# Kernel optimization log

Hardware: AMD Instinct MI355X
Metric: run time of the kernel (lower is better)

The kernel has to match this reference:

```python
import jax, jax.numpy as jnp
import numpy as np

B, N, C, NH = 4, 4096, 192, 3
H = W = 64
HD = C // NH  # 64
K_SPA = [8, 4, 2]
SCALE = C ** (-0.5)
LN_EPS = 1e-5


def _ln(x, g, b):
    m = jnp.mean(x, axis=-1, keepdims=True)
    v = jnp.mean(jnp.square(x - m), axis=-1, keepdims=True)
    return (x - m) * jax.lax.rsqrt(v + LN_EPS) * g + b


def _conv2d(x, w, b, padding='VALID', groups=1):
    y = jax.lax.conv_general_dilated(
        x, w, window_strides=(1, 1), padding=padding,
        dimension_numbers=('NCHW', 'OIHW', 'NCHW'), feature_group_count=groups)
    return y + b[None, :, None, None]


def _branch(x_img, q_h, kv_w, kv_b, sr_w, sr_b, ln_g, ln_b, lc_w, lc_b):
    # x_img: [B,C,H,W]; q_h: [B,N,HD]
    f = _conv2d(x_img, sr_w, sr_b)                      # [B,C,h',w'] (VALID, stride 1)
    m = f.shape[2] * f.shape[3]
    side = f.shape[2]                                   # square: h'==w'
    t = f.reshape(B, C, m).transpose(0, 2, 1)           # [B,m,C]
    t = jax.nn.gelu(_ln(t, ln_g, ln_b), approximate=False)
    kv = (t @ kv_w.T + kv_b).reshape(B, m, NH, HD)      # head-split of kv proj
    k = kv[:, :, 0, :]                                  # [B,m,HD] (head 0 -> k)
    v = kv[:, :, 1, :]                                  # [B,m,HD] (head 1 -> v)
    attn = jax.nn.softmax(jnp.einsum('bnd,bmd->bnm', q_h, k) * SCALE, axis=-1)
    v_img = v.transpose(0, 2, 1).reshape(B, HD, side, side)
    v = v + _conv2d(v_img, lc_w, lc_b, padding=((1, 1), (1, 1)), groups=HD)\
        .reshape(B, HD, m).transpose(0, 2, 1)           # local depthwise conv added to V
    return jnp.einsum('bnm,bmd->bnd', attn, v)          # [B,N,HD]


def _fwd(x, q_w, q_b, kv_w, kv_b, sr1_w, sr1_b, sr2_w, sr2_b, sr3_w, sr3_b,
         ln1_g, ln1_b, ln2_g, ln2_b, ln3_g, ln3_b,
         lc1_w, lc1_b, lc2_w, lc2_b, lc3_w, lc3_b, nn1_w, nn1_b):
    q = (x @ q_w.T + q_b).reshape(B, N, NH, HD).transpose(0, 2, 1, 3)  # [B,NH,N,HD]
    x_img = x.transpose(0, 2, 1).reshape(B, C, H, W)
    x1 = _branch(x_img, q[:, 0], kv_w, kv_b, sr1_w, sr1_b, ln1_g, ln1_b, lc1_w, lc1_b)
    x2 = _branch(x_img, q[:, 1], kv_w, kv_b, sr2_w, sr2_b, ln2_g, ln2_b, lc2_w, lc2_b)
    x3 = _branch(x_img, q[:, 2], kv_w, kv_b, sr3_w, sr3_b, ln3_g, ln3_b, lc3_w, lc3_b)
    out = jnp.concatenate([x1, x2, x3], axis=-1)        # [B,N,C]
    return out @ nn1_w.T + nn1_b


def setup_inputs() -> dict:
    key = jax.random.key(0)
    ks = jax.random.split(key, 16)
    s = lambda i, shp: (jax.random.normal(ks[i], shp, jnp.float32) * 0.02)
    d = dict(
        x=jax.random.normal(ks[0], (B, N, C), jnp.float32),
        q_w=s(1, (C, C)), q_b=jnp.zeros((C,), jnp.float32),
        kv_w=s(2, (C, C)), kv_b=jnp.zeros((C,), jnp.float32),
        sr1_w=s(3, (C, C, K_SPA[0], K_SPA[0])), sr1_b=jnp.zeros((C,), jnp.float32),
        sr2_w=s(4, (C, C, K_SPA[1], K_SPA[1])), sr2_b=jnp.zeros((C,), jnp.float32),
        sr3_w=s(5, (C, C, K_SPA[2], K_SPA[2])), sr3_b=jnp.zeros((C,), jnp.float32),
        ln1_g=jnp.ones((C,), jnp.float32), ln1_b=jnp.zeros((C,), jnp.float32),
        ln2_g=jnp.ones((C,), jnp.float32), ln2_b=jnp.zeros((C,), jnp.float32),
        ln3_g=jnp.ones((C,), jnp.float32), ln3_b=jnp.zeros((C,), jnp.float32),
        lc1_w=s(6, (HD, 1, 3, 3)), lc1_b=jnp.zeros((HD,), jnp.float32),
        lc2_w=s(7, (HD, 1, 3, 3)), lc2_b=jnp.zeros((HD,), jnp.float32),
        lc3_w=s(8, (HD, 1, 3, 3)), lc3_b=jnp.zeros((HD,), jnp.float32),
        nn1_w=s(9, (C, C)), nn1_b=jnp.zeros((C,), jnp.float32),
    )
    return d


def reference(x, q_w, q_b, kv_w, kv_b, sr1_w, sr1_b, sr2_w, sr2_b, sr3_w, sr3_b,
              ln1_g, ln1_b, ln2_g, ln2_b, ln3_g, ln3_b,
              lc1_w, lc1_b, lc2_w, lc2_b, lc3_w, lc3_b, nn1_w, nn1_b):
    return _fwd(x, q_w, q_b, kv_w, kv_b, sr1_w, sr1_b, sr2_w, sr2_b, sr3_w, sr3_b,
                ln1_g, ln1_b, ln2_g, ln2_b, ln3_g, ln3_b,
                lc1_w, lc1_b, lc2_w, lc2_b, lc3_w, lc3_b, nn1_w, nn1_b)
```

## Files before the change

### kernel.cpp

```cpp
#include <hip/hip_runtime.h>
#include <hip/hip_bf16.h>

typedef unsigned short u16;
typedef unsigned int   u32;
typedef __attribute__((ext_vector_type(8))) short bf16x8;
typedef __attribute__((ext_vector_type(4))) float f32x4;

#define DI static __device__ __forceinline__
#define MFMA(a,b,c) __builtin_amdgcn_mfma_f32_16x16x32_bf16(a,b,c,0,0,0)

static constexpr int CB = 192;
static constexpr int NB = 4096;
static constexpr int BB = 4;
static constexpr float SCALE = 0.07216878364870323f;

DI float b2f(u16 u){ union{u32 i; float f;} x; x.i = (u32)u << 16; return x.f; }
DI u16 f2b(float f){ union{u32 i; float f;} x; x.f = f;
  u32 r = x.i + 0x7FFFu + ((x.i >> 16) & 1u); return (u16)(r >> 16); }

DI int swzb(int row, int byteInRow){ return row*128 + (byteInRow ^ ((row & 7) << 4)); }

template<bool F32>
DI void stage16(const void* base, size_t eoff, char* dst, int srow, int q4){
  if (F32){
    const float* s = (const float*)base + eoff;
    float4 a0 = *(const float4*)(s);
    float4 a1 = *(const float4*)(s + 4);
    float4 a2 = *(const float4*)(s + 8);
    float4 a3 = *(const float4*)(s + 12);
    union { uint4 v; u16 h[8]; } r0, r1;
    r0.h[0]=f2b(a0.x); r0.h[1]=f2b(a0.y); r0.h[2]=f2b(a0.z); r0.h[3]=f2b(a0.w);
    r0.h[4]=f2b(a1.x); r0.h[5]=f2b(a1.y); r0.h[6]=f2b(a1.z); r0.h[7]=f2b(a1.w);
    r1.h[0]=f2b(a2.x); r1.h[1]=f2b(a2.y); r1.h[2]=f2b(a2.z); r1.h[3]=f2b(a2.w);
    r1.h[4]=f2b(a3.x); r1.h[5]=f2b(a3.y); r1.h[6]=f2b(a3.z); r1.h[7]=f2b(a3.w);
    *(uint4*)(dst + swzb(srow, q4*32))      = r0.v;
    *(uint4*)(dst + swzb(srow, q4*32 + 16)) = r1.v;
  } else {
    const u16* s = (const u16*)base + eoff;
    *(uint4*)(dst + swzb(srow, q4*32))      = *(const uint4*)(s);
    *(uint4*)(dst + swzb(srow, q4*32 + 16)) = *(const uint4*)(s + 8);
  }
}

__global__ __launch_bounds__(256) void cvt_k(const float* __restrict__ in,
      u16* __restrict__ out, int n4){
  int i = blockIdx.x*256 + threadIdx.x;
  if (i >= n4) return;
  float4 v = ((const float4*)in)[i];
  union{ uint2 u; u16 h[4]; } r;
  r.h[0]=f2b(v.x); r.h[1]=f2b(v.y); r.h[2]=f2b(v.z); r.h[3]=f2b(v.w);
  ((uint2*)out)[i] = r.u;
}

template<int K>
__global__ void repack_k(const float* __restrict__ w, u16* __restrict__ wt, int total){
  int i = blockIdx.x*256 + threadIdx.x;
  if (i >= total) return;
  int kk  = i / (CB*CB);
  int rem = i % (CB*CB);
  int co = rem / CB, ci = rem % CB;
  int ky = kk / K, kx = kk % K;
  wt[i] = f2b(w[((co*CB + ci)*K + ky)*K + kx]);
}

template<int K>
__global__ __launch_bounds__(256) void conv_k(const u16* __restrict__ xb,
      const u16* __restrict__ wt, const float* __restrict__ bias,
      u16* __restrict__ out, int side, int m){
  constexpr int AR = K*64;
  __shared__ char lds[(AR + 2*192)*128];
  char* Awin = lds;
  char* W0 = lds + AR*128;
  char* W1 = W0 + 192*128;

  const int t = threadIdx.x;
  const int w = t >> 6, l = t & 63, lr = l & 15, lg = l >> 4;
  const int b = blockIdx.x / side;
  const int oy = blockIdx.x % side;

  int boff[12][2];
  #pragma unroll
  for (int f = 0; f < 12; ++f){
    boff[f][0] = swzb(16*f + lr, lg*16);
    boff[f][1] = swzb(16*f + lr, 64 + lg*16);
  }

  f32x4 zero = {0.f,0.f,0.f,0.f};
  f32x4 acc[12];
  #pragma unroll
  for (int f = 0; f < 12; ++f) acc[f] = zero;

  const int rowb = 16*w + lr;
  const int scol = t >> 2, sq4 = t & 3;

  for (int c0 = 0; c0 < CB; c0 += 64){
    __syncthreads();
    #pragma unroll
    for (int r = 0; r < K; ++r){
      stage16<false>(xb, ((size_t)(b*NB + (oy + r)*64 + scol))*CB + c0 + sq4*16,
                     Awin, r*64 + scol, sq4);
    }
    #pragma unroll
    for (int k = 0; k < 3; ++k){
      int s = t + k*256, row = s >> 2, q4 = s & 3;
      stage16<false>(wt, ((size_t)row)*CB + c0 + q4*16, W0, row, q4);
    }
    for (int kk = 0; kk < K*K; ++kk){
      __syncthreads();
      char* Wcur = (kk & 1) ? W1 : W0;
      if (kk + 1 < K*K){
        char* Wnxt = (kk & 1) ? W0 : W1;
        #pragma unroll
        for (int k = 0; k < 3; ++k){
          int s = t + k*256, row = s >> 2, q4 = s & 3;
          stage16<false>(wt, ((size_t)(kk+1)*CB + row)*CB + c0 + q4*16, Wnxt, row, q4);
        }
      }
      int ky = kk / K, kx = kk - ky*K;
      int arow = ky*64 + rowb + kx;
      int x16 = (arow & 7) << 4;
      const char* ab = Awin + arow*128;
      bf16x8 a0 = *(const bf16x8*)(ab + ((lg*16) ^ x16));
      bf16x8 a1 = *(const bf16x8*)(ab + ((64 + lg*16) ^ x16));
      #pragma unroll
      for (int f = 0; f < 12; ++f){
        bf16x8 b0v = *(const bf16x8*)(Wcur + boff[f][0]);
        bf16x8 b1v = *(const bf16x8*)(Wcur + boff[f][1]);
        acc[f] = MFMA(a0, b0v, acc[f]);
        acc[f] = MFMA(a1, b1v, acc[f]);
      }
    }
  }

  const int posb = oy*side;
  #pragma unroll
  for (int f = 0; f < 12; ++f){
    int co = 16*f + lr;
    float bv = bias[co];
    #pragma unroll
    for (int r = 0; r < 4; ++r){
      int ox = 16*w + lg*4 + r;
      if (ox < side)
        out[((size_t)(b*m + posb + ox))*CB + co] = f2b(acc[f][r] + bv);
    }
  }
}

struct GemmP {
  const void* A; const void* W; const float* bias;
  u16* outb; u16* outk; u16* outv; float* outf;
  int Mtot;
  int m;
  int mtiles, ntiles;
};

template<int EPI, bool AF32, bool WF32>
__global__ __launch_bounds__(256) void gemm_k(GemmP p){
  __shared__ uint4 ldsbuf[1024];
  char* ldsA = (char*)ldsbuf;
  char* ldsB = ldsA + 8192;

  const int t = threadIdx.x;
  const int w = t >> 6, l = t & 63, lr = l & 15, lg = l >> 4;

  int bid = blockIdx.x;
  int nt = bid % p.ntiles, mt = bid / p.ntiles;

  const int srow = t >> 2;
  const int q4   = t & 3;

  size_t abase;
  { int row = mt*64 + srow; if (row > p.Mtot - 1) row = p.Mtot - 1;
    abase = (size_t)row * CB; }
  const int wrow = nt*64 + srow;

  const int aoff0 = swzb(16*w + lr, lg*16);
  const int aoff1 = swzb(16*w + lr, 64 + lg*16);
  int boff[4][2];
  #pragma unroll
  for (int f = 0; f < 4; ++f){ boff[f][0] = swzb(16*f + lr, lg*16); boff[f][1] = swzb(16*f + lr, 64 + lg*16); }

  f32x4 zero = {0.f,0.f,0.f,0.f};
  f32x4 acc[4] = {zero, zero, zero, zero};

  size_t wbase = (size_t)wrow * CB;
  for (int c0 = 0; c0 < CB; c0 += 64){
    stage16<AF32>(p.A, abase + c0 + q4*16, ldsA, srow, q4);
    stage16<WF32>(p.W, wbase + c0 + q4*16, ldsB, srow, q4);
    __syncthreads();
    bf16x8 a0 = *(const bf16x8*)(ldsA + aoff0);
    bf16x8 a1 = *(const bf16x8*)(ldsA + aoff1);
    #pragma unroll
    for (int f = 0; f < 4; ++f){
      bf16x8 b0 = *(const bf16x8*)(ldsB + boff[f][0]);
      bf16x8 b1 = *(const bf16x8*)(ldsB + boff[f][1]);
      acc[f] = MFMA(a0, b0, acc[f]);
      acc[f] = MFMA(a1, b1, acc[f]);
    }
    __syncthreads();
  }

  #pragma unroll
  for (int f = 0; f < 4; ++f){
    #pragma unroll
    for (int r = 0; r < 4; ++r){
      int rowt = 16*w + lg*4 + r;
      int col  = nt*64 + 16*f + lr;
      float v = acc[f][r] + p.bias[col];
      int grow = mt*64 + rowt;
      if (grow >= p.Mtot) continue;
      if (EPI == 0){
        p.outb[(size_t)grow*CB + col] = f2b(v);
      } else if (EPI == 2){
        int bb = grow / p.m, pp = grow % p.m;
        if (col < 64) p.outk[(size_t)(bb*p.m + pp)*64 + col]        = f2b(v);
        else          p.outv[(size_t)(bb*p.m + pp)*64 + (col - 64)] = f2b(v);
      } else {
        p.outf[(size_t)grow*CB + col] = v;
      }
    }
  }
}

__global__ __launch_bounds__(256) void ln_gelu_k(const u16* __restrict__ tp,
      const float* __restrict__ g, const float* __restrict__ bt,
      u16* __restrict__ out, int rows){
  int w = threadIdx.x >> 6, l = threadIdx.x & 63;
  int p = blockIdx.x*4 + w;
  if (p >= rows) return;
  const u16* rp = tp + (size_t)p*CB;
  float x0 = b2f(rp[l]), x1 = b2f(rp[l+64]), x2 = b2f(rp[l+128]);
  float s = x0 + x1 + x2;
  #pragma unroll
  for (int d = 1; d < 64; d <<= 1) s += __shfl_xor(s, d);
  float mean = s * (1.0f/192.0f);
  float d0 = x0-mean, d1 = x1-mean, d2 = x2-mean;
  float q = d0*d0 + d1*d1 + d2*d2;
  #pragma unroll
  for (int d = 1; d < 64; d <<= 1) q += __shfl_xor(q, d);
  float rstd = rsqrtf(q * (1.0f/192.0f) + 1e-5f);
  u16* op = out + (size_t)p*CB;
  float dv[3] = {d0, d1, d2};
  #pragma unroll
  for (int i = 0; i < 3; ++i){
    int c = l + i*64;
    float xv = dv[i] * rstd * g[c] + bt[c];
    float ge = 0.5f * xv * (1.0f + erff(xv * 0.7071067811865475f));
    op[c] = f2b(ge);
  }
}

__global__ __launch_bounds__(256) void lcconv_k(const u16* __restrict__ vpre,
      const float* __restrict__ lw, const float* __restrict__ lb,
      u16* __restrict__ vt, int m, int mpad, int side){
  int w = threadIdx.x >> 6, d = threadIdx.x & 63;
  int idx = blockIdx.x*4 + w;
  if (idx >= BB*m) return;
  int b = idx / m, p = idx % m;
  int h = p / side, x = p % side;
  float acc = b2f(vpre[(size_t)idx*64 + d]);
  float wv[9];
  #pragma unroll
  for (int j = 0; j < 9; ++j) wv[j] = lw[d*9 + j];
  #pragma unroll
  for (int dy = 0; dy < 3; ++dy){
    int hh = h + dy - 1;
    if (hh < 0 || hh >= side) continue;
    #pragma unroll
    for (int dx = 0; dx < 3; ++dx){
      int ww = x + dx - 1;
      if (ww < 0 || ww >= side) continue;
      acc += b2f(vpre[(size_t)(b*m + hh*side + ww)*64 + d]) * wv[dy*3 + dx];
    }
  }
  acc += lb[d];
  vt[(size_t)(b*64 + d)*mpad + p] = f2b(acc);
}

__global__ __launch_bounds__(256) void attn_k(const u16* __restrict__ qall,
      const u16* __restrict__ kbuf, const u16* __restrict__ vt,
      u16* __restrict__ xh, int m, int mpad, int head){
  __shared__ uint4 lds[2048];
  char* Qb = (char*)lds;
  char* Kb = Qb + 8192;
  char* Vb = Kb + 8192;
  const int t = threadIdx.x;
  const int w = t >> 6, l = t & 63, lr = l & 15, lg = l >> 4;
  char* Pb = Vb + 8192 + w*2048;
  const int b = blockIdx.x >> 6, q0 = (blockIdx.x & 63)*64;

  {
    int row = t >> 2, seg = (t & 3)*32;
    const char* src = (const char*)(qall + (size_t)(b*NB + q0 + row)*CB + head*64) + seg;
    *(uint4*)(Qb + swzb(row, seg))    = *(const uint4*)src;
    *(uint4*)(Qb + swzb(row, seg+16)) = *(const uint4*)(src + 16);
  }

  const int qoff0 = swzb(16*w + lr, lg*16), qoff1 = swzb(16*w + lr, 64 + lg*16);
  int koff[4][2];
  #pragma unroll
  for (int f = 0; f < 4; ++f){ koff[f][0] = swzb(16*f + lr, lg*16); koff[f][1] = swzb(16*f + lr, 64 + lg*16); }
  const int poff0 = swzb(lr, lg*16), poff1 = swzb(lr, 64 + lg*16);

  float mrow[4] = {-1e30f,-1e30f,-1e30f,-1e30f};
  float lrow[4] = {0.f,0.f,0.f,0.f};
  f32x4 zero = {0.f,0.f,0.f,0.f};
  f32x4 oacc[4] = {zero, zero, zero, zero};

  const int nkc = (m + 63) / 64;
  for (int kc = 0; kc < nkc; ++kc){
    const int j0 = kc*64;
    __syncthreads();
    {
      int j = t >> 2, seg = (t & 3)*32;
      int jj = j0 + j; if (jj > m-1) jj = m-1;
      const char* src = (const char*)(kbuf + (size_t)(b*m + jj)*64) + seg;
      *(uint4*)(Kb + swzb(j, seg))    = *(const uint4*)src;
      *(uint4*)(Kb + swzb(j, seg+16)) = *(const uint4*)(src + 16);
      int d = j;
      const char* sv = (const char*)(vt + (size_t)(b*64 + d)*mpad + j0) + seg;
      *(uint4*)(Vb + swzb(d, seg))    = *(const uint4*)sv;
      *(uint4*)(Vb + swzb(d, seg+16)) = *(const uint4*)(sv + 16);
    }
    __syncthreads();

    f32x4 s[4] = {zero, zero, zero, zero};
    bf16x8 a0 = *(const bf16x8*)(Qb + qoff0);
    bf16x8 a1 = *(const bf16x8*)(Qb + qoff1);
    #pragma unroll
    for (int f = 0; f < 4; ++f){
      bf16x8 k0 = *(const bf16x8*)(Kb + koff[f][0]);
      bf16x8 k1 = *(const bf16x8*)(Kb + koff[f][1]);
      s[f] = MFMA(a0, k0, s[f]);
      s[f] = MFMA(a1, k1, s[f]);
    }
    float fac[4];
    #pragma unroll
    for (int r = 0; r < 4; ++r){
      float mx = -1e30f;
      #pragma unroll
      for (int f = 0; f < 4; ++f){
        float sv = s[f][r] * SCALE;
        int key = j0 + 16*f + lr;
        sv = (key < m) ? sv : -1e30f;
        s[f][r] = sv;
        mx = fmaxf(mx, sv);
      }
      mx = fmaxf(mx, __shfl_xor(mx, 1));
      mx = fmaxf(mx, __shfl_xor(mx, 2));
      mx = fmaxf(mx, __shfl_xor(mx, 4));
      mx = fmaxf(mx, __shfl_xor(mx, 8));
      float mold = mrow[r];
      float mnew = fmaxf(mold, mx);
      mrow[r] = mnew;
      fac[r] = __expf(mold - mnew);
      float rs = 0.f;
      #pragma unroll
      for (int f = 0; f < 4; ++f){
        float pe = __expf(s[f][r] - mnew);
        rs += pe;
        int prow = lg*4 + r, pcol = 16*f + lr;
        *(u16*)(Pb + swzb(prow, pcol*2)) = f2b(pe);
      }
      rs += __shfl_xor(rs, 1);
      rs += __shfl_xor(rs, 2);
      rs += __shfl_xor(rs, 4);
      rs += __shfl_xor(rs, 8);
      lrow[r] = lrow[r]*fac[r] + rs;
    }
    #pragma unroll
    for (int f = 0; f < 4; ++f){
      oacc[f][0] *= fac[0]; oacc[f][1] *= fac[1];
      oacc[f][2] *= fac[2]; oacc[f][3] *= fac[3];
    }
    __syncthreads();
    bf16x8 p0 = *(const bf16x8*)(Pb + poff0);
    bf16x8 p1 = *(const bf16x8*)(Pb + poff1);
    #pragma unroll
    for (int f = 0; f < 4; ++f){
      bf16x8 v0 = *(const bf16x8*)(Vb + koff[f][0]);
      bf16x8 v1 = *(const bf16x8*)(Vb + koff[f][1]);
      oacc[f] = MFMA(p0, v0, oacc[f]);
      oacc[f] = MFMA(p1, v1, oacc[f]);
    }
  }

  #pragma unroll
  for (int f = 0; f < 4; ++f){
    #pragma unroll
    for (int r = 0; r < 4; ++r){
      int row = q0 + 16*w + lg*4 + r;
      int col = head*64 + 16*f + lr;
      xh[(size_t)(b*NB + row)*CB + col] = f2b(oacc[f][r] / lrow[r]);
    }
  }
}

extern "C" void kernel_launch(void* const* d_in, const int* in_sizes, int n_in,
                              void* d_out, int out_size, void* d_ws, size_t ws_size,
                              hipStream_t stream){
  const float* x     = (const float*)d_in[0];
  const float* q_w   = (const float*)d_in[1];
  const float* q_b   = (const float*)d_in[2];
  const float* kv_w  = (const float*)d_in[3];
  const float* kv_b  = (const float*)d_in[4];
  const float* sr_w[3] = {(const float*)d_in[5], (const float*)d_in[7], (const float*)d_in[9]};
  const float* sr_b[3] = {(const float*)d_in[6], (const float*)d_in[8], (const float*)d_in[10]};
  const float* ln_g[3] = {(const float*)d_in[11], (const float*)d_in[13], (const float*)d_in[15]};
  const float* ln_b[3] = {(const float*)d_in[12], (const float*)d_in[14], (const float*)d_in[16]};
  const float* lc_w[3] = {(const float*)d_in[17], (const float*)d_in[19], (const float*)d_in[21]};
  const float* lc_b[3] = {(const float*)d_in[18], (const float*)d_in[20], (const float*)d_in[22]};
  const float* nn1_w = (const float*)d_in[23];
  const float* nn1_b = (const float*)d_in[24];

  char* ws = (char*)d_ws;
  u16* q_all  = (u16*)d_out;
  u16* xb     = (u16*)(ws);
  u16* xheads = (u16*)(ws + 6291456);
  u16* wt     = (u16*)(ws + 12582912);
  u16* kbuf   = (u16*)(ws + 12582912);
  u16* vpre   = (u16*)(ws + 14615040);
  u16* tpre   = (u16*)(ws + 17301504);
  u16* vtb    = (u16*)(ws + 17301504);
  u16* tbuf   = (u16*)(ws + 23397888);

  const int Ks[3] = {8, 4, 2}, sides[3] = {57, 61, 63};

  cvt_k<<<3072, 256, 0, stream>>>(x, xb, 786432);

  {
    GemmP p{}; p.A = xb; p.W = q_w; p.bias = q_b; p.outb = q_all;
    p.Mtot = BB*NB; p.m = BB*NB; p.mtiles = 256; p.ntiles = 3;
    gemm_k<0,false,true><<<256*3, 256, 0, stream>>>(p);
  }

  for (int i = 0; i < 3; ++i){
    const int K = Ks[i], side = sides[i], m = side*side;
    const int mpad = ((m + 64 + 7)/8)*8;
    const int tot = CB*CB*K*K;
    if (i == 0) repack_k<8><<<(tot+255)/256, 256, 0, stream>>>(sr_w[i], wt, tot);
    if (i == 1) repack_k<4><<<(tot+255)/256, 256, 0, stream>>>(sr_w[i], wt, tot);
    if (i == 2) repack_k<2><<<(tot+255)/256, 256, 0, stream>>>(sr_w[i], wt, tot);

    if (i == 0) conv_k<8><<<BB*side, 256, 0, stream>>>(xb, wt, sr_b[i], tpre, side, m);
    if (i == 1) conv_k<4><<<BB*side, 256, 0, stream>>>(xb, wt, sr_b[i], tpre, side, m);
    if (i == 2) conv_k<2><<<BB*side, 256, 0, stream>>>(xb, wt, sr_b[i], tpre, side, m);

    ln_gelu_k<<<m, 256, 0, stream>>>(tpre, ln_g[i], ln_b[i], tbuf, BB*m);

    GemmP pk{}; pk.A = tbuf; pk.W = kv_w; pk.bias = kv_b; pk.outk = kbuf; pk.outv = vpre;
    pk.Mtot = BB*m; pk.m = m; pk.mtiles = (BB*m + 63)/64; pk.ntiles = 2;
    gemm_k<2,false,true><<<pk.mtiles*2, 256, 0, stream>>>(pk);

    lcconv_k<<<m, 256, 0, stream>>>(vpre, lc_w[i], lc_b[i], vtb, m, mpad, side);

    attn_k<<<BB*64, 256, 0, stream>>>(q_all, kbuf, vtb, xheads, m, mpad, i);
  }

  {
    GemmP p{}; p.A = xheads; p.W = nn1_w; p.bias = nn1_b; p.outf = (float*)d_out;
    p.Mtot = BB*NB; p.m = BB*NB; p.mtiles = 256; p.ntiles = 3;
    gemm_k<3,false,true><<<256*3, 256, 0, stream>>>(p);
  }
}
```

Measured before the change: 790.6 us.

## Double block size in conv and attention kernels, splitting work across wave groups

```diff
diff --git a/kernel.cpp b/kernel.cpp
--- a/kernel.cpp
+++ b/kernel.cpp
@@ -64,7 +64,7 @@
 }
 
 template<int K>
-__global__ __launch_bounds__(256) void conv_k(const u16* __restrict__ xb,
+__global__ __launch_bounds__(512) void conv_k(const u16* __restrict__ xb,
       const u16* __restrict__ wt, const float* __restrict__ bias,
       u16* __restrict__ out, int side, int m){
   constexpr int AR = K*64;
@@ -74,36 +74,44 @@
   char* W1 = W0 + 192*128;
 
   const int t = threadIdx.x;
-  const int w = t >> 6, l = t & 63, lr = l & 15, lg = l >> 4;
+  const int l = t & 63, lr = l & 15, lg = l >> 4;
+  const int ww = (t >> 6) & 3, wg = t >> 8;
   const int b = blockIdx.x / side;
   const int oy = blockIdx.x % side;
 
-  int boff[12][2];
-  #pragma unroll
-  for (int f = 0; f < 12; ++f){
-    boff[f][0] = swzb(16*f + lr, lg*16);
-    boff[f][1] = swzb(16*f + lr, 64 + lg*16);
+  int boff[6][2];
+  #pragma unroll
+  for (int f = 0; f < 6; ++f){
+    boff[f][0] = swzb(96*wg + 16*f + lr, lg*16);
+    boff[f][1] = swzb(96*wg + 16*f + lr, 64 + lg*16);
   }
 
   f32x4 zero = {0.f,0.f,0.f,0.f};
-  f32x4 acc[12];
-  #pragma unroll
-  for (int f = 0; f < 12; ++f) acc[f] = zero;
-
-  const int rowb = 16*w + lr;
-  const int scol = t >> 2, sq4 = t & 3;
+  f32x4 acc[6];
+  #pragma unroll
+  for (int f = 0; f < 6; ++f) acc[f] = zero;
+
+  const int rowb = 16*ww + lr;
 
   for (int c0 = 0; c0 < CB; c0 += 64){
     __syncthreads();
     #pragma unroll
-    for (int r = 0; r < K; ++r){
-      stage16<false>(xb, ((size_t)(b*NB + (oy + r)*64 + scol))*CB + c0 + sq4*16,
-                     Awin, r*64 + scol, sq4);
-    }
-    #pragma unroll
-    for (int k = 0; k < 3; ++k){
-      int s = t + k*256, row = s >> 2, q4 = s & 3;
-      stage16<false>(wt, ((size_t)row)*CB + c0 + q4*16, W0, row, q4);
+    for (int k = 0; k < (K*256 + 511)/512; ++k){
+      int s = t + k*512;
+      if (s < K*256){
+        int row = s >> 2, q4 = s & 3;
+        int r = row >> 6, scol = row & 63;
+        stage16<false>(xb, ((size_t)(b*NB + (oy + r)*64 + scol))*CB + c0 + q4*16,
+                       Awin, row, q4);
+      }
+    }
+    #pragma unroll
+    for (int k = 0; k < 2; ++k){
+      int s = t + k*512;
+      if (s < 768){
+        int row = s >> 2, q4 = s & 3;
+        stage16<false>(wt, ((size_t)row)*CB + c0 + q4*16, W0, row, q4);
+      }
     }
     for (int kk = 0; kk < K*K; ++kk){
       __syncthreads();
@@ -111,9 +119,12 @@
       if (kk + 1 < K*K){
         char* Wnxt = (kk & 1) ? W0 : W1;
         #pragma unroll
-        for (int k = 0; k < 3; ++k){
-          int s = t + k*256, row = s >> 2, q4 = s & 3;
-          stage16<false>(wt, ((size_t)(kk+1)*CB + row)*CB + c0 + q4*16, Wnxt, row, q4);
+        for (int k = 0; k < 2; ++k){
+          int s = t + k*512;
+          if (s < 768){
+            int row = s >> 2, q4 = s & 3;
+            stage16<false>(wt, ((size_t)(kk+1)*CB + row)*CB + c0 + q4*16, Wnxt, row, q4);
+          }
         }
       }
       int ky = kk / K, kx = kk - ky*K;
@@ -123,7 +134,7 @@
       bf16x8 a0 = *(const bf16x8*)(ab + ((lg*16) ^ x16));
       bf16x8 a1 = *(const bf16x8*)(ab + ((64 + lg*16) ^ x16));
       #pragma unroll
-      for (int f = 0; f < 12; ++f){
+      for (int f = 0; f < 6; ++f){
         bf16x8 b0v = *(const bf16x8*)(Wcur + boff[f][0]);
         bf16x8 b1v = *(const bf16x8*)(Wcur + boff[f][1]);
         acc[f] = MFMA(a0, b0v, acc[f]);
@@ -134,12 +145,12 @@
 
   const int posb = oy*side;
   #pragma unroll
-  for (int f = 0; f < 12; ++f){
-    int co = 16*f + lr;
+  for (int f = 0; f < 6; ++f){
+    int co = 96*wg + 16*f + lr;
     float bv = bias[co];
     #pragma unroll
     for (int r = 0; r < 4; ++r){
-      int ox = 16*w + lg*4 + r;
+      int ox = 16*ww + lg*4 + r;
       if (ox < side)
         out[((size_t)(b*m + posb + ox))*CB + co] = f2b(acc[f][r] + bv);
     }
@@ -277,26 +288,30 @@
   vt[(size_t)(b*64 + d)*mpad + p] = f2b(acc);
 }
 
-__global__ __launch_bounds__(256) void attn_k(const u16* __restrict__ qall,
+__global__ __launch_bounds__(512) void attn_k(const u16* __restrict__ qall,
       const u16* __restrict__ kbuf, const u16* __restrict__ vt,
       u16* __restrict__ xh, int m, int mpad, int head){
-  __shared__ uint4 lds[2048];
-  char* Qb = (char*)lds;
-  char* Kb = Qb + 8192;
-  char* Vb = Kb + 8192;
+  __shared__ char lds[57344];
+  char* Qb = lds;
+  char* Kb = lds + 8192;
+  char* Vb = lds + 24576;
+  char* Pb = lds + 40960;
   const int t = threadIdx.x;
   const int w = t >> 6, l = t & 63, lr = l & 15, lg = l >> 4;
-  char* Pb = Vb + 8192 + w*2048;
+  const int ww = w & 3, wg = w >> 2;
+  char* Kg = Kb + wg*8192;
+  char* Vg = Vb + wg*8192;
+  char* Pw = Pb + w*2048;
   const int b = blockIdx.x >> 6, q0 = (blockIdx.x & 63)*64;
 
-  {
+  if (t < 256){
     int row = t >> 2, seg = (t & 3)*32;
     const char* src = (const char*)(qall + (size_t)(b*NB + q0 + row)*CB + head*64) + seg;
     *(uint4*)(Qb + swzb(row, seg))    = *(const uint4*)src;
     *(uint4*)(Qb + swzb(row, seg+16)) = *(const uint4*)(src + 16);
   }
 
-  const int qoff0 = swzb(16*w + lr, lg*16), qoff1 = swzb(16*w + lr, 64 + lg*16);
+  const int qoff0 = swzb(16*ww + lr, lg*16), qoff1 = swzb(16*ww + lr, 64 + lg*16);
   int koff[4][2];
   #pragma unroll
   for (int f = 0; f < 4; ++f){ koff[f][0] = swzb(16*f + lr, lg*16); koff[f][1] = swzb(16*f + lr, 64 + lg*16); }
@@ -308,90 +323,120 @@
   f32x4 oacc[4] = {zero, zero, zero, zero};
 
   const int nkc = (m + 63) / 64;
-  for (int kc = 0; kc < nkc; ++kc){
+  const int cmax = (nkc + 1) >> 1;
+  const int tt = t & 255;
+  for (int it = 0; it < cmax; ++it){
+    const int kc = it*2 + wg;
+    const bool active = kc < nkc;
     const int j0 = kc*64;
     __syncthreads();
-    {
-      int j = t >> 2, seg = (t & 3)*32;
+    if (active){
+      int j = tt >> 2, seg = (tt & 3)*32;
       int jj = j0 + j; if (jj > m-1) jj = m-1;
       const char* src = (const char*)(kbuf + (size_t)(b*m + jj)*64) + seg;
-      *(uint4*)(Kb + swzb(j, seg))    = *(const uint4*)src;
-      *(uint4*)(Kb + swzb(j, seg+16)) = *(const uint4*)(src + 16);
+      *(uint4*)(Kg + swzb(j, seg))    = *(const uint4*)src;
+      *(uint4*)(Kg + swzb(j, seg+16)) = *(const uint4*)(src + 16);
       int d = j;
       const char* sv = (const char*)(vt + (size_t)(b*64 + d)*mpad + j0) + seg;
-      *(uint4*)(Vb + swzb(d, seg))    = *(const uint4*)sv;
-      *(uint4*)(Vb + swzb(d, seg+16)) = *(const uint4*)(sv + 16);
+      *(uint4*)(Vg + swzb(d, seg))    = *(const uint4*)sv;
+      *(uint4*)(Vg + swzb(d, seg+16)) = *(const uint4*)(sv + 16);
     }
     __syncthreads();
-
-    f32x4 s[4] = {zero, zero, zero, zero};
-    bf16x8 a0 = *(const bf16x8*)(Qb + qoff0);
-    bf16x8 a1 = *(const bf16x8*)(Qb + qoff1);
-    #pragma unroll
-    for (int f = 0; f < 4; ++f){
-      bf16x8 k0 = *(const bf16x8*)(Kb + koff[f][0]);
-      bf16x8 k1 = *(const bf16x8*)(Kb + koff[f][1]);
-      s[f] = MFMA(a0, k0, s[f]);
-      s[f] = MFMA(a1, k1, s[f]);
-    }
-    float fac[4];
-    #pragma unroll
-    for (int r = 0; r < 4; ++r){
-      float mx = -1e30f;
+    if (active){
+      f32x4 s[4] = {zero, zero, zero, zero};
+      bf16x8 a0 = *(const bf16x8*)(Qb + qoff0);
+      bf16x8 a1 = *(const bf16x8*)(Qb + qoff1);
       #pragma unroll
       for (int f = 0; f < 4; ++f){
-        float sv = s[f][r] * SCALE;
-        int key = j0 + 16*f + lr;
-        sv = (key < m) ? sv : -1e30f;
-        s[f][r] = sv;
-        mx = fmaxf(mx, sv);
-      }
-      mx = fmaxf(mx, __shfl_xor(mx, 1));
-      mx = fmaxf(mx, __shfl_xor(mx, 2));
-      mx = fmaxf(mx, __shfl_xor(mx, 4));
-      mx = fmaxf(mx, __shfl_xor(mx, 8));
-      float mold = mrow[r];
-      float mnew = fmaxf(mold, mx);
-      mrow[r] = mnew;
-      fac[r] = __expf(mold - mnew);
-      float rs = 0.f;
+        bf16x8 k0 = *(const bf16x8*)(Kg + koff[f][0]);
+        bf16x8 k1 = *(const bf16x8*)(Kg + koff[f][1]);
+        s[f] = MFMA(a0, k0, s[f]);
+        s[f] = MFMA(a1, k1, s[f]);
+      }
+      float fac[4];
+      #pragma unroll
+      for (int r = 0; r < 4; ++r){
+        float mx = -1e30f;
+        #pragma unroll
+        for (int f = 0; f < 4; ++f){
+          float sv = s[f][r] * SCALE;
+          int key = j0 + 16*f + lr;
+          sv = (key < m) ? sv : -1e30f;
+          s[f][r] = sv;
+          mx = fmaxf(mx, sv);
+        }
+        mx = fmaxf(mx, __shfl_xor(mx, 1));
+        mx = fmaxf(mx, __shfl_xor(mx, 2));
+        mx = fmaxf(mx, __shfl_xor(mx, 4));
+        mx = fmaxf(mx, __shfl_xor(mx, 8));
+        float mold = mrow[r];
+        float mnew = fmaxf(mold, mx);
+        mrow[r] = mnew;
+        fac[r] = __expf(mold - mnew);
+        float rs = 0.f;
+        #pragma unroll
+        for (int f = 0; f < 4; ++f){
+          float pe = __expf(s[f][r] - mnew);
+          rs += pe;
+          int prow = lg*4 + r, pcol = 16*f + lr;
+          *(u16*)(Pw + swzb(prow, pcol*2)) = f2b(pe);
+        }
+        rs += __shfl_xor(rs, 1);
+        rs += __shfl_xor(rs, 2);
+        rs += __shfl_xor(rs, 4);
+        rs += __shfl_xor(rs, 8);
+        lrow[r] = lrow[r]*fac[r] + rs;
+      }
       #pragma unroll
       for (int f = 0; f < 4; ++f){
-        float pe = __expf(s[f][r] - mnew);
-        rs += pe;
-        int prow = lg*4 + r, pcol = 16*f + lr;
-        *(u16*)(Pb + swzb(prow, pcol*2)) = f2b(pe);
-      }
-      rs += __shfl_xor(rs, 1);
-      rs += __shfl_xor(rs, 2);
-      rs += __shfl_xor(rs, 4);
-      rs += __shfl_xor(rs, 8);
-      lrow[r] = lrow[r]*fac[r] + rs;
-    }
-    #pragma unroll
-    for (int f = 0; f < 4; ++f){
-      oacc[f][0] *= fac[0]; oacc[f][1] *= fac[1];
-      oacc[f][2] *= fac[2]; oacc[f][3] *= fac[3];
+        oacc[f][0] *= fac[0]; oacc[f][1] *= fac[1];
+        oacc[f][2] *= fac[2]; oacc[f][3] *= fac[3];
+      }
     }
     __syncthreads();
-    bf16x8 p0 = *(const bf16x8*)(Pb + poff0);
-    bf16x8 p1 = *(const bf16x8*)(Pb + poff1);
-    #pragma unroll
-    for (int f = 0; f < 4; ++f){
-      bf16x8 v0 = *(const bf16x8*)(Vb + koff[f][0]);
-      bf16x8 v1 = *(const bf16x8*)(Vb + koff[f][1]);
-      oacc[f] = MFMA(p0, v0, oacc[f]);
-      oacc[f] = MFMA(p1, v1, oacc[f]);
-    }
-  }
-
-  #pragma unroll
-  for (int f = 0; f < 4; ++f){
+    if (active){
+      bf16x8 p0 = *(const bf16x8*)(Pw + poff0);
+      bf16x8 p1 = *(const bf16x8*)(Pw + poff1);
+      #pragma unroll
+      for (int f = 0; f < 4; ++f){
+        bf16x8 v0 = *(const bf16x8*)(Vg + koff[f][0]);
+        bf16x8 v1 = *(const bf16x8*)(Vg + koff[f][1]);
+        oacc[f] = MFMA(p0, v0, oacc[f]);
+        oacc[f] = MFMA(p1, v1, oacc[f]);
+      }
+    }
+  }
+
+  __syncthreads();
+  if (wg == 1){
+    char* Mb = Kb + ww*6144;
+    #pragma unroll
+    for (int f = 0; f < 4; ++f) *(f32x4*)(Mb + l*64 + f*16) = oacc[f];
+    float4 mm = {mrow[0], mrow[1], mrow[2], mrow[3]};
+    *(float4*)(Mb + 4096 + l*16) = mm;
+    float4 ll = {lrow[0], lrow[1], lrow[2], lrow[3]};
+    *(float4*)(Mb + 5120 + l*16) = ll;
+  }
+  __syncthreads();
+  if (wg == 0){
+    char* Mb = Kb + ww*6144;
+    float4 m1 = *(const float4*)(Mb + 4096 + l*16);
+    float4 l1 = *(const float4*)(Mb + 5120 + l*16);
+    float M1[4] = {m1.x, m1.y, m1.z, m1.w};
+    float L1[4] = {l1.x, l1.y, l1.z, l1.w};
     #pragma unroll
     for (int r = 0; r < 4; ++r){
-      int row = q0 + 16*w + lg*4 + r;
-      int col = head*64 + 16*f + lr;
-      xh[(size_t)(b*NB + row)*CB + col] = f2b(oacc[f][r] / lrow[r]);
+      float M = fmaxf(mrow[r], M1[r]);
+      float e0 = __expf(mrow[r] - M), e1 = __expf(M1[r] - M);
+      float lt = lrow[r]*e0 + L1[r]*e1;
+      #pragma unroll
+      for (int f = 0; f < 4; ++f){
+        float o1 = ((const f32x4*)(Mb + l*64 + f*16))[0][r];
+        float val = (oacc[f][r]*e0 + o1*e1) / lt;
+        int row = q0 + 16*ww + lg*4 + r;
+        int col = head*64 + 16*f + lr;
+        xh[(size_t)(b*NB + row)*CB + col] = f2b(val);
+      }
     }
   }
 }
@@ -442,9 +487,9 @@
     if (i == 1) repack_k<4><<<(tot+255)/256, 256, 0, stream>>>(sr_w[i], wt, tot);
     if (i == 2) repack_k<2><<<(tot+255)/256, 256, 0, stream>>>(sr_w[i], wt, tot);
 
-    if (i == 0) conv_k<8><<<BB*side, 256, 0, stream>>>(xb, wt, sr_b[i], tpre, side, m);
-    if (i == 1) conv_k<4><<<BB*side, 256, 0, stream>>>(xb, wt, sr_b[i], tpre, side, m);
-    if (i == 2) conv_k<2><<<BB*side, 256, 0, stream>>>(xb, wt, sr_b[i], tpre, side, m);
+    if (i == 0) conv_k<8><<<BB*side, 512, 0, stream>>>(xb, wt, sr_b[i], tpre, side, m);
+    if (i == 1) conv_k<4><<<BB*side, 512, 0, stream>>>(xb, wt, sr_b[i], tpre, side, m);
+    if (i == 2) conv_k<2><<<BB*side, 512, 0, stream>>>(xb, wt, sr_b[i], tpre, side, m);
 
     ln_gelu_k<<<m, 256, 0, stream>>>(tpre, ln_g[i], ln_b[i], tbuf, BB*m);
 
@@ -454,7 +499,7 @@
 
     lcconv_k<<<m, 256, 0, stream>>>(vpre, lc_w[i], lc_b[i], vtb, m, mpad, side);
 
-    attn_k<<<BB*64, 256, 0, stream>>>(q_all, kbuf, vtb, xheads, m, mpad, i);
+    attn_k<<<BB*64, 512, 0, stream>>>(q_all, kbuf, vtb, xheads, m, mpad, i);
   }
 
   {
```

Result: faster. 702.3 us (-11.2%).
